# Kernel optimization log

Hardware: AMD Instinct MI355X
Metric: run time of the kernel (lower is better)

Reference implementation:

```python
import jax, jax.numpy as jnp
import numpy as np

H = 90          # hidden size
T = 240         # timesteps
F = 180         # encoder input features (3*60)


def _lstmcell_zero_state(x, W_ih, b_ih, b_hh):
    """nn.LSTMCell applied with h0=c0=0 (as in the original loops).
    x: [..., in_feat]; W_ih: [4H, in_feat]. Gate order i,f,g,o (PyTorch)."""
    gates = jnp.einsum('btf,gf->btg', x, W_ih) + b_ih + b_hh  # [B,T,4H]
    i, f, g, o = jnp.split(gates, 4, axis=-1)
    c = jax.nn.sigmoid(i) * jnp.tanh(g)          # f * c0 term vanishes (c0=0)
    return jax.nn.sigmoid(o) * jnp.tanh(c)       # h'


def setup_inputs() -> dict:
    key = jax.random.key(0)
    ks = jax.random.split(key, 9)
    s_enc = 1.0 / np.sqrt(H)
    inp = {
        'x': jax.random.normal(ks[0], (1024, 3, 60, T), dtype=jnp.float32),
        'enc_W_ih': jax.random.uniform(ks[1], (4 * H, F), jnp.float32, -s_enc, s_enc),
        'enc_b_ih': jax.random.uniform(ks[2], (4 * H,), jnp.float32, -s_enc, s_enc),
        'enc_b_hh': jax.random.uniform(ks[3], (4 * H,), jnp.float32, -s_enc, s_enc),
        'dec_W_ih': jax.random.uniform(ks[4], (4 * H, H), jnp.float32, -s_enc, s_enc),
        'dec_b_ih': jax.random.uniform(ks[5], (4 * H,), jnp.float32, -s_enc, s_enc),
        'dec_b_hh': jax.random.uniform(ks[6], (4 * H,), jnp.float32, -s_enc, s_enc),
        'out_W': jax.random.uniform(ks[7], (40, T * H), jnp.float32, -1.0 / np.sqrt(T * H), 1.0 / np.sqrt(T * H)),
        'out_b': jax.random.uniform(ks[8], (40,), jnp.float32, -1.0 / np.sqrt(T * H), 1.0 / np.sqrt(T * H)),
    }
    return inp


def reference(x, enc_W_ih, enc_b_ih, enc_b_hh, dec_W_ih, dec_b_ih, dec_b_hh, out_W, out_b):
    # Encoder: [B,3,60,240] -> [B,240,180]
    xe = jnp.transpose(x, (0, 3, 1, 2)).reshape(-1, T, F)
    h1 = jax.nn.sigmoid(_lstmcell_zero_state(xe, enc_W_ih, enc_b_ih, enc_b_hh))  # [B,T,90]
    # Decoder: per-step LSTMCell (also zero-state each step)
    h2 = _lstmcell_zero_state(h1, dec_W_ih, dec_b_ih, dec_b_hh)  # [B,T,90]
    out = h2.reshape(-1, T * H) @ out_W.T + out_b                # [B,40]
    out = out.reshape(-1, 4, 10)
    return jax.nn.softmax(out, axis=2)
```

## Files before the change

kernel.cpp:

```cpp
#include <hip/hip_runtime.h>
#include <hip/hip_bf16.h>

#define TT 240
#define FEAT 180
#define HID 90

typedef __attribute__((ext_vector_type(8))) short bf16x8;
typedef __attribute__((ext_vector_type(4))) short s16x4;
typedef __attribute__((ext_vector_type(4))) float f32x4;

static __device__ __forceinline__ short f2bf(float f) {
    union { float f; unsigned int u; } c; c.f = f;
    return (short)((c.u + 0x8000u) >> 16);
}
static __device__ __forceinline__ float fexp2(float x) { return __builtin_amdgcn_exp2f(x); }
static __device__ __forceinline__ float frcp(float x)  { return __builtin_amdgcn_rcpf(x); }
#define LOG2E 1.4426950408889634f
static __device__ __forceinline__ float sigm(float x)  { return frcp(1.f + fexp2(-LOG2E * x)); }
static __device__ __forceinline__ float tanh_(float x) { return 2.f * frcp(1.f + fexp2(-2.f * LOG2E * x)) - 1.f; }
static __device__ __forceinline__ unsigned int pk2(float lo, float hi) {
    return (unsigned int)(unsigned short)f2bf(lo) | ((unsigned int)(unsigned short)f2bf(hi) << 16);
}

__global__ __launch_bounds__(256) void k_prep(
    const float* __restrict__ outW, const float* __restrict__ encW,
    const float* __restrict__ decW,
    short* __restrict__ woutB, short* __restrict__ wencP, short* __restrict__ wdecP)
{
    int idx = blockIdx.x * 256 + threadIdx.x;
    if (idx < 129600) {
        int row = idx / 2700, v = idx - row * 2700;
        uint4 w = {0u, 0u, 0u, 0u};
        if (row < 40) {
            const float* s = outW + row * 21600 + v * 8;
            f32x4 a = *(const f32x4*)(s);
            f32x4 b = *(const f32x4*)(s + 4);
            w.x = pk2(a[0], a[1]); w.y = pk2(a[2], a[3]);
            w.z = pk2(b[0], b[1]); w.w = pk2(b[2], b[3]);
        }
        *(uint4*)(woutB + row * 21600 + v * 8) = w;
        return;
    }
    idx -= 129600;
    if (idx < 288 * 192) {
        int row = idx / 192, k = idx - row * 192;
        int gi = row / 96, h = row - gi * 96;
        float v = 0.f;
        if (h < 90 && k < 180) {
            int srow = (gi == 0 ? 0 : (gi == 1 ? 180 : 270)) + h;
            v = encW[srow * 180 + k];
        }
        wencP[idx] = f2bf(v);
        return;
    }
    idx -= 288 * 192;
    if (idx < 288 * 96) {
        int row = idx / 96, k = idx - row * 96;
        int gi = row / 96, h = row - gi * 96;
        float v = 0.f;
        if (h < 90 && k < 90) {
            int srow = (gi == 0 ? 0 : (gi == 1 ? 180 : 270)) + h;
            v = decW[srow * 90 + k];
        }
        wdecP[idx] = f2bf(v);
    }
}

__global__ __launch_bounds__(384) void k_ed(
    const float* __restrict__ x,
    const short* __restrict__ wencP, const short* __restrict__ wdecP,
    const float* __restrict__ eb_ih, const float* __restrict__ eb_hh,
    const float* __restrict__ db_ih, const float* __restrict__ db_hh,
    short* __restrict__ h2)
{
    __shared__ short As[64][200];
    __shared__ short Hs[64][104];
    const int tid  = threadIdx.x;
    const int lane = tid & 63;
    const int wv   = tid >> 6;
    const int b    = blockIdx.x >> 2;
    const int q    = blockIdx.x & 3;
    const int r15  = lane & 15;
    const int k8   = lane >> 4;
    const int rbase = k8 * 4;

    bf16x8 wfE[3][6];
    #pragma unroll
    for (int g = 0; g < 3; ++g) {
        const short* wp = wencP + (g * 96 + wv * 16 + r15) * 192 + k8 * 8;
        #pragma unroll
        for (int kk = 0; kk < 6; ++kk) wfE[g][kk] = *(const bf16x8*)(wp + kk * 32);
    }
    const int h  = wv * 16 + r15;
    const int hc = (h < 90) ? h : 89;
    const float bIe = eb_ih[hc] + eb_hh[hc];
    const float bGe = eb_ih[180 + hc] + eb_hh[180 + hc];
    const float bOe = eb_ih[270 + hc] + eb_hh[270 + hc];
    const float bId = db_ih[hc] + db_hh[hc];
    const float bGd = db_ih[180 + hc] + db_hh[180 + hc];
    const float bOd = db_ih[270 + hc] + db_hh[270 + hc];

    {
        int row = tid / 6, u = tid - row * 6;
        *(unsigned int*)(&As[row][180 + u * 2]) = 0u;
        if (tid < 360) {
            int r = 60 + tid / 90, c2 = (tid - (tid / 90) * 90) * 2;
            *(unsigned int*)(&As[r][c2]) = 0u;
        }
    }

    {
        const float* xs = x + b * 43200 + q * 60;
        #pragma unroll
        for (int it = 0; it < 2; ++it) {
            int task = tid + 384 * it;
            if (task < 675) {
                int fb = task / 15, v = task - fb * 15;
                const float* p = xs + (fb * 4) * 240 + v * 4;
                f32x4 L0 = *(const f32x4*)(p);
                f32x4 L1 = *(const f32x4*)(p + 240);
                f32x4 L2 = *(const f32x4*)(p + 480);
                f32x4 L3 = *(const f32x4*)(p + 720);
                #pragma unroll
                for (int i = 0; i < 4; ++i) {
                    s16x4 w = { f2bf(L0[i]), f2bf(L1[i]), f2bf(L2[i]), f2bf(L3[i]) };
                    *(s16x4*)(&As[v * 4 + i][fb * 4]) = w;
                }
            }
        }
    }
    __syncthreads();

    #pragma unroll
    for (int rs = 0; rs < 4; ++rs) {
        f32x4 aI = {0.f,0.f,0.f,0.f}, aG = {0.f,0.f,0.f,0.f}, aO = {0.f,0.f,0.f,0.f};
        #pragma unroll
        for (int kk = 0; kk < 6; ++kk) {
            bf16x8 a = *(const bf16x8*)(&As[rs * 16 + r15][kk * 32 + k8 * 8]);
            aI = __builtin_amdgcn_mfma_f32_16x16x32_bf16(a, wfE[0][kk], aI, 0, 0, 0);
            aG = __builtin_amdgcn_mfma_f32_16x16x32_bf16(a, wfE[1][kk], aG, 0, 0, 0);
            aO = __builtin_amdgcn_mfma_f32_16x16x32_bf16(a, wfE[2][kk], aO, 0, 0, 0);
        }
        #pragma unroll
        for (int rg = 0; rg < 4; ++rg) {
            float c  = sigm(aI[rg] + bIe) * tanh_(aG[rg] + bGe);
            float hv = sigm(aO[rg] + bOe) * tanh_(c);
            Hs[rs * 16 + rbase + rg][h] = f2bf(sigm(hv));
        }
    }
    __syncthreads();

    bf16x8 wfD[3][3];
    #pragma unroll
    for (int g = 0; g < 3; ++g) {
        const short* wp = wdecP + (g * 96 + wv * 16 + r15) * 96 + k8 * 8;
        #pragma unroll
        for (int kk = 0; kk < 3; ++kk) wfD[g][kk] = *(const bf16x8*)(wp + kk * 32);
    }

    short* h2s = &As[0][0];
    #pragma unroll
    for (int rs = 0; rs < 4; ++rs) {
        f32x4 aI = {0.f,0.f,0.f,0.f}, aG = {0.f,0.f,0.f,0.f}, aO = {0.f,0.f,0.f,0.f};
        #pragma unroll
        for (int kk = 0; kk < 3; ++kk) {
            bf16x8 a = *(const bf16x8*)(&Hs[rs * 16 + r15][kk * 32 + k8 * 8]);
            aI = __builtin_amdgcn_mfma_f32_16x16x32_bf16(a, wfD[0][kk], aI, 0, 0, 0);
            aG = __builtin_amdgcn_mfma_f32_16x16x32_bf16(a, wfD[1][kk], aG, 0, 0, 0);
            aO = __builtin_amdgcn_mfma_f32_16x16x32_bf16(a, wfD[2][kk], aO, 0, 0, 0);
        }
        #pragma unroll
        for (int rg = 0; rg < 4; ++rg) {
            float c  = sigm(aI[rg] + bId) * tanh_(aG[rg] + bGd);
            float o2 = sigm(aO[rg] + bOd) * tanh_(c);
            h2s[(rs * 16 + rbase + rg) * 96 + h] = f2bf(o2);
        }
    }
    __syncthreads();

    unsigned int* hp = (unsigned int*)(h2 + (size_t)b * 21600 + q * 5400);
    #pragma unroll
    for (int i = 0; i < 8; ++i) {
        int idx = tid + 384 * i;
        if (idx < 2700) {
            int r = idx / 45, c = idx - r * 45;
            hp[idx] = *(const unsigned int*)(&h2s[r * 96 + c * 2]);
        }
    }
}

#define KSPLIT 135
#define KCH    5
__global__ __launch_bounds__(64) void k_out(
    const short* __restrict__ h2, const short* __restrict__ woutB,
    float* __restrict__ part, int B)
{
    const int MT  = B >> 4;
    const int bid = blockIdx.x;
    const int kc  = bid / MT;
    const int mt  = bid - kc * MT;
    const int lane = threadIdx.x & 63;
    const int r15  = lane & 15;
    const int k8   = lane >> 4;

    const int row = mt * 16 + r15;
    const short* aB = h2    + (size_t)row * 21600 + kc * (KCH * 32) + k8 * 8;
    const short* bB = woutB + (size_t)r15 * 21600 + kc * (KCH * 32) + k8 * 8;

    f32x4 a0 = {0.f,0.f,0.f,0.f}, a1 = {0.f,0.f,0.f,0.f}, a2 = {0.f,0.f,0.f,0.f};
    #pragma unroll
    for (int ks = 0; ks < KCH; ++ks) {
        bf16x8 a  = *(const bf16x8*)(aB + ks * 32);
        bf16x8 q0 = *(const bf16x8*)(bB + ks * 32);
        bf16x8 q1 = *(const bf16x8*)(bB + 16 * 21600 + ks * 32);
        bf16x8 q2 = *(const bf16x8*)(bB + 32 * 21600 + ks * 32);
        a0 = __builtin_amdgcn_mfma_f32_16x16x32_bf16(a, q0, a0, 0, 0, 0);
        a1 = __builtin_amdgcn_mfma_f32_16x16x32_bf16(a, q1, a1, 0, 0, 0);
        a2 = __builtin_amdgcn_mfma_f32_16x16x32_bf16(a, q2, a2, 0, 0, 0);
    }
    float* pb = part + ((size_t)kc * B + mt * 16) * 48;
    #pragma unroll
    for (int rg = 0; rg < 4; ++rg) {
        int r = k8 * 4 + rg;
        pb[r * 48 +      r15] = a0[rg];
        pb[r * 48 + 16 + r15] = a1[rg];
        pb[r * 48 + 32 + r15] = a2[rg];
    }
}

__global__ __launch_bounds__(256) void k_soft(
    const float* __restrict__ part, const float* __restrict__ outb,
    float* __restrict__ out, int B)
{
    const int b = blockIdx.x, tid = threadIdx.x;
    __shared__ float psum[240];
    __shared__ float vals[40];
    if (tid < 240) {
        int o = tid % 40, g = tid / 40;
        float s = 0.f;
        for (int kc = g; kc < KSPLIT; kc += 6)
            s += part[((size_t)kc * B + b) * 48 + o];
        psum[tid] = s;
    }
    __syncthreads();
    if (tid < 40) {
        float s = outb[tid];
        #pragma unroll
        for (int g = 0; g < 6; ++g) s += psum[tid + 40 * g];
        vals[tid] = s;
    }
    __syncthreads();
    if (tid < 4) {
        float mx = -1e30f;
        #pragma unroll
        for (int j = 0; j < 10; ++j) mx = fmaxf(mx, vals[tid * 10 + j]);
        float e[10], s = 0.f;
        #pragma unroll
        for (int j = 0; j < 10; ++j) { e[j] = fexp2(LOG2E * (vals[tid * 10 + j] - mx)); s += e[j]; }
        float inv = frcp(s);
        #pragma unroll
        for (int j = 0; j < 10; ++j) out[b * 40 + tid * 10 + j] = e[j] * inv;
    }
}

extern "C" void kernel_launch(void* const* d_in, const int* in_sizes, int n_in,
                              void* d_out, int out_size, void* d_ws, size_t ws_size,
                              hipStream_t stream)
{
    const float* x     = (const float*)d_in[0];
    const float* encW  = (const float*)d_in[1];
    const float* eb_ih = (const float*)d_in[2];
    const float* eb_hh = (const float*)d_in[3];
    const float* decW  = (const float*)d_in[4];
    const float* db_ih = (const float*)d_in[5];
    const float* db_hh = (const float*)d_in[6];
    const float* outW  = (const float*)d_in[7];
    const float* outb  = (const float*)d_in[8];
    float* out = (float*)d_out;

    const int B = in_sizes[0] / (3 * 60 * TT);

    char* ws = (char*)d_ws;
    short* woutB = (short*)ws;
    short* wencP = (short*)(ws + 2073600);
    short* wdecP = (short*)(ws + 2184192);
    short* h2    = (short*)(ws + 2239488);
    float* part  = (float*)(ws + 2239488 + (size_t)B * 43200);

    k_prep<<<dim3(831), dim3(256), 0, stream>>>(outW, encW, decW, woutB, wencP, wdecP);
    k_ed<<<dim3(B * 4), dim3(384), 0, stream>>>(x, wencP, wdecP, eb_ih, eb_hh,
                                                db_ih, db_hh, h2);
    k_out<<<dim3(KSPLIT * (B >> 4)), dim3(64), 0, stream>>>(h2, woutB, part, B);
    k_soft<<<dim3(B), dim3(256), 0, stream>>>(part, outb, out, B);
}
```

Measured before the change: 379.0 us.

## Stage output weights in LDS and drop separate Hs buffer in encoder kernel

The output projection kernel now uses 256-thread blocks covering 64 batch rows and a 480-wide K chunk. The weight slice for that chunk is staged once in shared memory and shared by four waves, instead of each 64-thread block re-reading the weights from global memory. The KSPLIT shrinks from 135 to 45, which cuts the partial-sum traffic handled by the softmax kernel. In the encoder/decoder kernel the separate Hs LDS array is removed: h1 and h2 values are held in registers and written back into the reused As buffer with extra barriers. This lowers LDS use per block, which may raise occupancy, at the cost of more synchronisation.

```diff
diff --git a/kernel.cpp b/kernel.cpp
--- a/kernel.cpp
+++ b/kernel.cpp
@@ -74,7 +74,6 @@
     short* __restrict__ h2)
 {
     __shared__ short As[64][200];
-    __shared__ short Hs[64][104];
     const int tid  = threadIdx.x;
     const int lane = tid & 63;
     const int wv   = tid >> 6;
@@ -131,6 +130,7 @@
     }
     __syncthreads();
 
+    short h1v[16];
     #pragma unroll
     for (int rs = 0; rs < 4; ++rs) {
         f32x4 aI = {0.f,0.f,0.f,0.f}, aG = {0.f,0.f,0.f,0.f}, aO = {0.f,0.f,0.f,0.f};
@@ -145,10 +145,14 @@
         for (int rg = 0; rg < 4; ++rg) {
             float c  = sigm(aI[rg] + bIe) * tanh_(aG[rg] + bGe);
             float hv = sigm(aO[rg] + bOe) * tanh_(c);
-            Hs[rs * 16 + rbase + rg][h] = f2bf(sigm(hv));
-        }
-    }
-    __syncthreads();
+            h1v[rs * 4 + rg] = f2bf(sigm(hv));
+        }
+    }
+    __syncthreads();
+
+    #pragma unroll
+    for (int j = 0; j < 16; ++j)
+        As[(j >> 2) * 16 + rbase + (j & 3)][h] = h1v[j];
 
     bf16x8 wfD[3][3];
     #pragma unroll
@@ -157,14 +161,15 @@
         #pragma unroll
         for (int kk = 0; kk < 3; ++kk) wfD[g][kk] = *(const bf16x8*)(wp + kk * 32);
     }
-
-    short* h2s = &As[0][0];
+    __syncthreads();
+
+    short h2v[16];
     #pragma unroll
     for (int rs = 0; rs < 4; ++rs) {
         f32x4 aI = {0.f,0.f,0.f,0.f}, aG = {0.f,0.f,0.f,0.f}, aO = {0.f,0.f,0.f,0.f};
         #pragma unroll
         for (int kk = 0; kk < 3; ++kk) {
-            bf16x8 a = *(const bf16x8*)(&Hs[rs * 16 + r15][kk * 32 + k8 * 8]);
+            bf16x8 a = *(const bf16x8*)(&As[rs * 16 + r15][kk * 32 + k8 * 8]);
             aI = __builtin_amdgcn_mfma_f32_16x16x32_bf16(a, wfD[0][kk], aI, 0, 0, 0);
             aG = __builtin_amdgcn_mfma_f32_16x16x32_bf16(a, wfD[1][kk], aG, 0, 0, 0);
             aO = __builtin_amdgcn_mfma_f32_16x16x32_bf16(a, wfD[2][kk], aO, 0, 0, 0);
@@ -173,9 +178,15 @@
         for (int rg = 0; rg < 4; ++rg) {
             float c  = sigm(aI[rg] + bId) * tanh_(aG[rg] + bGd);
             float o2 = sigm(aO[rg] + bOd) * tanh_(c);
-            h2s[(rs * 16 + rbase + rg) * 96 + h] = f2bf(o2);
-        }
-    }
+            h2v[rs * 4 + rg] = f2bf(o2);
+        }
+    }
+    __syncthreads();
+
+    short* h2s = &As[0][0];
+    #pragma unroll
+    for (int j = 0; j < 16; ++j)
+        h2s[((j >> 2) * 16 + rbase + (j & 3)) * 96 + h] = h2v[j];
     __syncthreads();
 
     unsigned int* hp = (unsigned int*)(h2 + (size_t)b * 21600 + q * 5400);
@@ -189,36 +200,50 @@
     }
 }
 
-#define KSPLIT 135
-#define KCH    5
-__global__ __launch_bounds__(64) void k_out(
+#define KSPLIT 45
+#define KST    15
+__global__ __launch_bounds__(256) void k_out(
     const short* __restrict__ h2, const short* __restrict__ woutB,
     float* __restrict__ part, int B)
 {
-    const int MT  = B >> 4;
+    __shared__ short Bs[48][488];
+    const int MT  = B >> 6;
     const int bid = blockIdx.x;
     const int kc  = bid / MT;
     const int mt  = bid - kc * MT;
-    const int lane = threadIdx.x & 63;
-    const int r15  = lane & 15;
-    const int k8   = lane >> 4;
-
-    const int row = mt * 16 + r15;
-    const short* aB = h2    + (size_t)row * 21600 + kc * (KCH * 32) + k8 * 8;
-    const short* bB = woutB + (size_t)r15 * 21600 + kc * (KCH * 32) + k8 * 8;
+    const int tid = threadIdx.x;
+
+    {
+        const int k0 = kc * 480;
+        #pragma unroll
+        for (int j = 0; j < 12; ++j) {
+            int g = tid + 256 * j;
+            if (g < 2880) {
+                int r = g / 60, c = g - r * 60;
+                *(uint4*)(&Bs[r][c * 8]) =
+                    *(const uint4*)(woutB + (size_t)r * 21600 + k0 + c * 8);
+            }
+        }
+    }
+    __syncthreads();
+
+    const int w = tid >> 6, lane = tid & 63;
+    const int r15 = lane & 15, k8 = lane >> 4;
+    const int row = mt * 64 + w * 16 + r15;
+    const short* aB = h2 + (size_t)row * 21600 + kc * 480 + k8 * 8;
 
     f32x4 a0 = {0.f,0.f,0.f,0.f}, a1 = {0.f,0.f,0.f,0.f}, a2 = {0.f,0.f,0.f,0.f};
-    #pragma unroll
-    for (int ks = 0; ks < KCH; ++ks) {
+    #pragma unroll 5
+    for (int ks = 0; ks < KST; ++ks) {
         bf16x8 a  = *(const bf16x8*)(aB + ks * 32);
-        bf16x8 q0 = *(const bf16x8*)(bB + ks * 32);
-        bf16x8 q1 = *(const bf16x8*)(bB + 16 * 21600 + ks * 32);
-        bf16x8 q2 = *(const bf16x8*)(bB + 32 * 21600 + ks * 32);
+        bf16x8 q0 = *(const bf16x8*)(&Bs[r15][ks * 32 + k8 * 8]);
+        bf16x8 q1 = *(const bf16x8*)(&Bs[16 + r15][ks * 32 + k8 * 8]);
+        bf16x8 q2 = *(const bf16x8*)(&Bs[32 + r15][ks * 32 + k8 * 8]);
         a0 = __builtin_amdgcn_mfma_f32_16x16x32_bf16(a, q0, a0, 0, 0, 0);
         a1 = __builtin_amdgcn_mfma_f32_16x16x32_bf16(a, q1, a1, 0, 0, 0);
         a2 = __builtin_amdgcn_mfma_f32_16x16x32_bf16(a, q2, a2, 0, 0, 0);
     }
-    float* pb = part + ((size_t)kc * B + mt * 16) * 48;
+    float* pb = part + ((size_t)kc * B + mt * 64 + w * 16) * 48;
     #pragma unroll
     for (int rg = 0; rg < 4; ++rg) {
         int r = k8 * 4 + rg;
@@ -290,6 +315,6 @@
     k_prep<<<dim3(831), dim3(256), 0, stream>>>(outW, encW, decW, woutB, wencP, wdecP);
     k_ed<<<dim3(B * 4), dim3(384), 0, stream>>>(x, wencP, wdecP, eb_ih, eb_hh,
                                                 db_ih, db_hh, h2);
-    k_out<<<dim3(KSPLIT * (B >> 4)), dim3(64), 0, stream>>>(h2, woutB, part, B);
+    k_out<<<dim3(KSPLIT * (B >> 6)), dim3(256), 0, stream>>>(h2, woutB, part, B);
     k_soft<<<dim3(B), dim3(256), 0, stream>>>(part, outb, out, B);
 }
```

After: 361.1 us. 1.05x faster.
